# Kernel tuning notes

Measured on AMD Instinct MI355X. Metric: run time of the kernel, lower is better.

## Reference

```python
import jax, jax.numpy as jnp
import numpy as np

N = 8192
LAYER_WIDTHS = [32, 64, 32]
LAYER_CENTERS = [512, 512]


def setup_inputs() -> dict:
    key = jax.random.key(0)
    ks = jax.random.split(key, 8)
    inp = {"x": jax.random.normal(ks[0], (N, LAYER_WIDTHS[0]), dtype=jnp.float32)}
    # layer 0 params
    inp["centers0"] = jax.random.normal(ks[1], (LAYER_CENTERS[0], LAYER_WIDTHS[0]), dtype=jnp.float32)
    inp["log_sigmas0"] = jnp.zeros((LAYER_CENTERS[0],), dtype=jnp.float32)
    lim0 = 1.0 / np.sqrt(LAYER_CENTERS[0])
    inp["W0"] = jax.random.uniform(ks[2], (LAYER_WIDTHS[1], LAYER_CENTERS[0]), jnp.float32, -lim0, lim0)
    inp["b0"] = jax.random.uniform(ks[3], (LAYER_WIDTHS[1],), jnp.float32, -lim0, lim0)
    # layer 1 params
    inp["centers1"] = jax.random.normal(ks[4], (LAYER_CENTERS[1], LAYER_WIDTHS[1]), dtype=jnp.float32)
    inp["log_sigmas1"] = jnp.zeros((LAYER_CENTERS[1],), dtype=jnp.float32)
    lim1 = 1.0 / np.sqrt(LAYER_CENTERS[1])
    inp["W1"] = jax.random.uniform(ks[5], (LAYER_WIDTHS[2], LAYER_CENTERS[1]), jnp.float32, -lim1, lim1)
    inp["b1"] = jax.random.uniform(ks[6], (LAYER_WIDTHS[2],), jnp.float32, -lim1, lim1)
    return inp


def _rbf(h, centers, log_sigmas):
    # h: [N, in], centers: [C, in] -> [N, C]
    diff = h[:, None, :] - centers[None, :, :]            # [N, C, in]
    dist = jnp.sqrt(jnp.sum(diff * diff, axis=-1))        # [N, C]
    d = dist / jnp.exp(log_sigmas)[None, :]
    return jnp.exp(-(d * d))                              # gaussian basis


def reference(x, centers0, log_sigmas0, W0, b0, centers1, log_sigmas1, W1, b1):
    h = _rbf(x, centers0, log_sigmas0) @ W0.T + b0        # [N, widths[1]]
    h = _rbf(h, centers1, log_sigmas1) @ W1.T + b1        # [N, widths[2]]
    return h
```

## Files before the change

kernel.cpp:

```cpp
#include <hip/hip_runtime.h>
#include <math.h>


#define NROWS 8192
#define BLOCK 512
#define GRID (NROWS / 16)

typedef __attribute__((ext_vector_type(8))) short short8;
typedef __attribute__((ext_vector_type(4))) float f32x4;

__device__ __forceinline__ short bf16t(float f) {
    return (short)(__float_as_uint(f) >> 16);
}

__global__ void prepack(const float* __restrict__ c0, const float* __restrict__ ls0,
                        const float* __restrict__ W0,
                        const float* __restrict__ c1, const float* __restrict__ ls1,
                        const float* __restrict__ W1,
                        unsigned short* __restrict__ wpc0, unsigned short* __restrict__ wpc1,
                        unsigned short* __restrict__ wpw0, unsigned short* __restrict__ wpw1,
                        float2* __restrict__ cniv0, float2* __restrict__ cniv1)
{
    const int i = blockIdx.x * 256 + threadIdx.x;
    if (i < 16384) {
        const int e = i & 7, l = (i >> 3) & 63, nt = i >> 9;
        const int c = nt * 16 + (l & 15), k = (l >> 4) * 8 + e;
        wpc0[i] = (unsigned short)bf16t(c0[c * 32 + k]);
    } else if (i < 49152) {
        const int j = i - 16384;
        const int e = j & 7, l = (j >> 3) & 63, kk = (j >> 9) & 1, nt = j >> 10;
        const int c = nt * 16 + (l & 15), k = kk * 32 + (l >> 4) * 8 + e;
        wpc1[j] = (unsigned short)bf16t(c1[c * 64 + k]);
    } else if (i < 81920) {
        const int j = i - 49152;
        const int e = j & 7, l = (j >> 3) & 63, nt = (j >> 9) & 3, ks = j >> 11;
        const int col = nt * 16 + (l & 15), k = ks * 32 + (l >> 4) * 8 + e;
        wpw0[j] = (unsigned short)bf16t(W0[col * 512 + k]);
    } else if (i < 98304) {
        const int j = i - 81920;
        const int e = j & 7, l = (j >> 3) & 63, nt = (j >> 9) & 1, ks = j >> 10;
        const int col = nt * 16 + (l & 15), k = ks * 32 + (l >> 4) * 8 + e;
        wpw1[j] = (unsigned short)bf16t(W1[col * 512 + k]);
    } else if (i < 98304 + 512) {
        const int c = i - 98304;
        float s = 0.f;
        for (int d = 0; d < 32; ++d) { const float v = c0[c * 32 + d]; s += v * v; }
        cniv0[c] = make_float2(s, __expf(-2.0f * ls0[c]));
    } else if (i < 98304 + 1024) {
        const int c = i - 98816;
        float s = 0.f;
        for (int d = 0; d < 64; ++d) { const float v = c1[c * 64 + d]; s += v * v; }
        cniv1[c] = make_float2(s, __expf(-2.0f * ls1[c]));
    }
}

__global__ __launch_bounds__(BLOCK, 4)
void rbfnet(const float* __restrict__ x,
            const float* __restrict__ b0, const float* __restrict__ b1,
            const unsigned short* __restrict__ wpc0, const unsigned short* __restrict__ wpc1,
            const unsigned short* __restrict__ wpw0, const unsigned short* __restrict__ wpw1,
            const float2* __restrict__ cniv0, const float2* __restrict__ cniv1,
            float* __restrict__ out)
{
    __shared__ unsigned short phi_u[16 * 520];
    __shared__ unsigned short hfrag[16 * 72];
    __shared__ float htmp[2][16][68];
    __shared__ float otmp[4][16][36];
    __shared__ float hn_lds[16];

    const int t  = threadIdx.x;
    const int l  = t & 63;
    const int w  = t >> 6;
    const int mr = l & 15;
    const int kg = l >> 4;
    const int row0 = blockIdx.x * 16;

    short8 ax;
    float rnv[4];
    {
        const float4 x0 = *(const float4*)&x[(row0 + mr) * 32 + kg * 8];
        const float4 x1 = *(const float4*)&x[(row0 + mr) * 32 + kg * 8 + 4];
        const float xo[8] = {x0.x, x0.y, x0.z, x0.w, x1.x, x1.y, x1.z, x1.w};
        float rp = 0.f;
        #pragma unroll
        for (int i = 0; i < 8; ++i) { ax[i] = bf16t(xo[i]); rp += xo[i] * xo[i]; }
        rp += __shfl_xor(rp, 16);
        rp += __shfl_xor(rp, 32);
        #pragma unroll
        for (int g = 0; g < 4; ++g) rnv[g] = __shfl(rp, 4 * kg + g);
    }

    {
        #pragma unroll 2
        for (int q = 0; q < 4; ++q) {
            const int nt = 4 * w + q;
            const int c  = nt * 16 + mr;
            const short8 bc = *(const short8*)&wpc0[(nt * 64 + l) * 8];
            const float2 cv = cniv0[c];
            f32x4 d = {0.f, 0.f, 0.f, 0.f};
            d = __builtin_amdgcn_mfma_f32_16x16x32_bf16(ax, bc, d, 0, 0, 0);
            #pragma unroll
            for (int g = 0; g < 4; ++g) {
                const float p = __expf(-(rnv[g] + cv.x - 2.f * d[g]) * cv.y);
                phi_u[(4 * kg + g) * 520 + c] = (unsigned short)bf16t(p);
            }
        }
    }
    __syncthreads();

    {
        const int nt = w & 3, half = w >> 2;
        f32x4 hD = {0.f, 0.f, 0.f, 0.f};
        #pragma unroll 2
        for (int ks = 8 * half; ks < 8 * half + 8; ++ks) {
            const short8 ap = *(const short8*)&phi_u[mr * 520 + ks * 32 + kg * 8];
            const short8 bw = *(const short8*)&wpw0[((ks * 4 + nt) * 64 + l) * 8];
            hD = __builtin_amdgcn_mfma_f32_16x16x32_bf16(ap, bw, hD, 0, 0, 0);
        }
        #pragma unroll
        for (int g = 0; g < 4; ++g) htmp[half][4 * kg + g][nt * 16 + mr] = hD[g];
    }
    __syncthreads();

    {
        const int r = t >> 5, dd = t & 31;
        const float h0 = htmp[0][r][dd]      + htmp[1][r][dd]      + b0[dd];
        const float h1 = htmp[0][r][dd + 32] + htmp[1][r][dd + 32] + b0[dd + 32];
        hfrag[r * 72 + dd]      = (unsigned short)bf16t(h0);
        hfrag[r * 72 + 32 + dd] = (unsigned short)bf16t(h1);
        float s = h0 * h0 + h1 * h1;
        s += __shfl_xor(s, 1);  s += __shfl_xor(s, 2);  s += __shfl_xor(s, 4);
        s += __shfl_xor(s, 8);  s += __shfl_xor(s, 16);
        if (dd == 0) hn_lds[r] = s;
    }
    __syncthreads();

    {
        const short8 ah0 = *(const short8*)&hfrag[mr * 72 + kg * 8];
        const short8 ah1 = *(const short8*)&hfrag[mr * 72 + 32 + kg * 8];
        float hnv[4];
        #pragma unroll
        for (int g = 0; g < 4; ++g) hnv[g] = hn_lds[4 * kg + g];
        #pragma unroll 2
        for (int q = 0; q < 4; ++q) {
            const int nt = 4 * w + q;
            const int c  = nt * 16 + mr;
            const short8 bc0 = *(const short8*)&wpc1[((nt * 2 + 0) * 64 + l) * 8];
            const short8 bc1 = *(const short8*)&wpc1[((nt * 2 + 1) * 64 + l) * 8];
            const float2 cv = cniv1[c];
            f32x4 d = {0.f, 0.f, 0.f, 0.f};
            d = __builtin_amdgcn_mfma_f32_16x16x32_bf16(ah0, bc0, d, 0, 0, 0);
            d = __builtin_amdgcn_mfma_f32_16x16x32_bf16(ah1, bc1, d, 0, 0, 0);
            #pragma unroll
            for (int g = 0; g < 4; ++g) {
                const float p = __expf(-(hnv[g] + cv.x - 2.f * d[g]) * cv.y);
                phi_u[(4 * kg + g) * 520 + c] = (unsigned short)bf16t(p);
            }
        }
    }
    __syncthreads();

    {
        const int nt = w & 1, qtr = w >> 1;
        f32x4 oD = {0.f, 0.f, 0.f, 0.f};
        #pragma unroll 2
        for (int ks = 4 * qtr; ks < 4 * qtr + 4; ++ks) {
            const short8 ap = *(const short8*)&phi_u[mr * 520 + ks * 32 + kg * 8];
            const short8 bw = *(const short8*)&wpw1[((ks * 2 + nt) * 64 + l) * 8];
            oD = __builtin_amdgcn_mfma_f32_16x16x32_bf16(ap, bw, oD, 0, 0, 0);
        }
        #pragma unroll
        for (int g = 0; g < 4; ++g) otmp[qtr][4 * kg + g][nt * 16 + mr] = oD[g];
    }
    __syncthreads();

    {
        const int r = t >> 5, j = t & 31;
        const float s = otmp[0][r][j] + otmp[1][r][j] + otmp[2][r][j] + otmp[3][r][j] + b1[j];
        out[(row0 + r) * 32 + j] = s;
    }
}

extern "C" void kernel_launch(void* const* d_in, const int* in_sizes, int n_in,
                              void* d_out, int out_size, void* d_ws, size_t ws_size,
                              hipStream_t stream) {
    const float* xin = (const float*)d_in[0];
    const float* c0  = (const float*)d_in[1];
    const float* ls0 = (const float*)d_in[2];
    const float* W0  = (const float*)d_in[3];
    const float* b0  = (const float*)d_in[4];
    const float* c1  = (const float*)d_in[5];
    const float* ls1 = (const float*)d_in[6];
    const float* W1  = (const float*)d_in[7];
    const float* b1  = (const float*)d_in[8];
    float* outp = (float*)d_out;

    char* ws = (char*)d_ws;
    unsigned short* wpc0 = (unsigned short*)(ws);
    unsigned short* wpc1 = (unsigned short*)(ws + 32768);
    unsigned short* wpw0 = (unsigned short*)(ws + 98304);
    unsigned short* wpw1 = (unsigned short*)(ws + 163840);
    float2* cniv0 = (float2*)(ws + 196608);
    float2* cniv1 = (float2*)(ws + 200704);

    hipLaunchKernelGGL(prepack, dim3(388), dim3(256), 0, stream,
                       c0, ls0, W0, c1, ls1, W1, wpc0, wpc1, wpw0, wpw1, cniv0, cniv1);
    hipLaunchKernelGGL(rbfnet, dim3(GRID), dim3(BLOCK), 0, stream,
                       xin, b0, b1, wpc0, wpc1, wpw0, wpw1, cniv0, cniv1, outp);
}
```

Baseline: 79.08 us.

## Process 32 rows per block, drop split-K reductions, vectorize weight prepack

```diff
diff --git a/kernel.cpp b/kernel.cpp
--- a/kernel.cpp
+++ b/kernel.cpp
@@ -3,14 +3,18 @@
 
 
 #define NROWS 8192
+#define ROWS 32
 #define BLOCK 512
-#define GRID (NROWS / 16)
+#define GRID (NROWS / ROWS)
 
 typedef __attribute__((ext_vector_type(8))) short short8;
 typedef __attribute__((ext_vector_type(4))) float f32x4;
 
 __device__ __forceinline__ short bf16t(float f) {
     return (short)(__float_as_uint(f) >> 16);
+}
+__device__ __forceinline__ float bf16f(short u) {
+    return __uint_as_float(((unsigned)(unsigned short)u) << 16);
 }
 
 __global__ void prepack(const float* __restrict__ c0, const float* __restrict__ ls0,
@@ -21,40 +25,65 @@
                         unsigned short* __restrict__ wpw0, unsigned short* __restrict__ wpw1,
                         float2* __restrict__ cniv0, float2* __restrict__ cniv1)
 {
-    const int i = blockIdx.x * 256 + threadIdx.x;
-    if (i < 16384) {
-        const int e = i & 7, l = (i >> 3) & 63, nt = i >> 9;
-        const int c = nt * 16 + (l & 15), k = (l >> 4) * 8 + e;
-        wpc0[i] = (unsigned short)bf16t(c0[c * 32 + k]);
-    } else if (i < 49152) {
-        const int j = i - 16384;
-        const int e = j & 7, l = (j >> 3) & 63, kk = (j >> 9) & 1, nt = j >> 10;
-        const int c = nt * 16 + (l & 15), k = kk * 32 + (l >> 4) * 8 + e;
-        wpc1[j] = (unsigned short)bf16t(c1[c * 64 + k]);
-    } else if (i < 81920) {
-        const int j = i - 49152;
-        const int e = j & 7, l = (j >> 3) & 63, nt = (j >> 9) & 3, ks = j >> 11;
-        const int col = nt * 16 + (l & 15), k = ks * 32 + (l >> 4) * 8 + e;
-        wpw0[j] = (unsigned short)bf16t(W0[col * 512 + k]);
-    } else if (i < 98304) {
-        const int j = i - 81920;
-        const int e = j & 7, l = (j >> 3) & 63, nt = (j >> 9) & 1, ks = j >> 10;
-        const int col = nt * 16 + (l & 15), k = ks * 32 + (l >> 4) * 8 + e;
-        wpw1[j] = (unsigned short)bf16t(W1[col * 512 + k]);
-    } else if (i < 98304 + 512) {
-        const int c = i - 98304;
-        float s = 0.f;
-        for (int d = 0; d < 32; ++d) { const float v = c0[c * 32 + d]; s += v * v; }
-        cniv0[c] = make_float2(s, __expf(-2.0f * ls0[c]));
-    } else if (i < 98304 + 1024) {
-        const int c = i - 98816;
-        float s = 0.f;
-        for (int d = 0; d < 64; ++d) { const float v = c1[c * 64 + d]; s += v * v; }
-        cniv1[c] = make_float2(s, __expf(-2.0f * ls1[c]));
-    }
-}
-
-__global__ __launch_bounds__(BLOCK, 4)
+    const int b  = blockIdx.x;
+    const int gi = b * 256 + threadIdx.x;
+    const int l  = gi & 63, mr = l & 15, kg = l >> 4;
+
+    if (b < 8) {
+        const int nt = gi >> 6;
+        const float4 v0 = *(const float4*)&c0[(nt * 16 + mr) * 32 + kg * 8];
+        const float4 v1 = *(const float4*)&c0[(nt * 16 + mr) * 32 + kg * 8 + 4];
+        const float o[8] = {v0.x, v0.y, v0.z, v0.w, v1.x, v1.y, v1.z, v1.w};
+        short8 p; float rp = 0.f;
+        #pragma unroll
+        for (int i = 0; i < 8; ++i) { p[i] = bf16t(o[i]); rp += o[i] * o[i]; }
+        *(short8*)&wpc0[(nt * 64 + l) * 8] = p;
+        rp += __shfl_xor(rp, 16);
+        rp += __shfl_xor(rp, 32);
+        if (kg == 0)
+            cniv0[nt * 16 + mr] = make_float2(rp, __expf(-2.0f * ls0[nt * 16 + mr]));
+    } else if (b < 16) {
+        const int i2 = gi - 2048;
+        const int nt = i2 >> 6;
+        float rp = 0.f;
+        #pragma unroll
+        for (int kk = 0; kk < 2; ++kk) {
+            const float4 v0 = *(const float4*)&c1[(nt * 16 + mr) * 64 + kk * 32 + kg * 8];
+            const float4 v1 = *(const float4*)&c1[(nt * 16 + mr) * 64 + kk * 32 + kg * 8 + 4];
+            const float o[8] = {v0.x, v0.y, v0.z, v0.w, v1.x, v1.y, v1.z, v1.w};
+            short8 p;
+            #pragma unroll
+            for (int i = 0; i < 8; ++i) { p[i] = bf16t(o[i]); rp += o[i] * o[i]; }
+            *(short8*)&wpc1[((nt * 2 + kk) * 64 + l) * 8] = p;
+        }
+        rp += __shfl_xor(rp, 16);
+        rp += __shfl_xor(rp, 32);
+        if (kg == 0)
+            cniv1[nt * 16 + mr] = make_float2(rp, __expf(-2.0f * ls1[nt * 16 + mr]));
+    } else if (b < 32) {
+        const int i2 = gi - 4096;
+        const int nt = (i2 >> 6) & 3, ks = i2 >> 8;
+        const float4 v0 = *(const float4*)&W0[(nt * 16 + mr) * 512 + ks * 32 + kg * 8];
+        const float4 v1 = *(const float4*)&W0[(nt * 16 + mr) * 512 + ks * 32 + kg * 8 + 4];
+        const float o[8] = {v0.x, v0.y, v0.z, v0.w, v1.x, v1.y, v1.z, v1.w};
+        short8 p;
+        #pragma unroll
+        for (int i = 0; i < 8; ++i) p[i] = bf16t(o[i]);
+        *(short8*)&wpw0[((ks * 4 + nt) * 64 + l) * 8] = p;
+    } else {
+        const int i2 = gi - 8192;
+        const int nt = (i2 >> 6) & 1, ks = i2 >> 7;
+        const float4 v0 = *(const float4*)&W1[(nt * 16 + mr) * 512 + ks * 32 + kg * 8];
+        const float4 v1 = *(const float4*)&W1[(nt * 16 + mr) * 512 + ks * 32 + kg * 8 + 4];
+        const float o[8] = {v0.x, v0.y, v0.z, v0.w, v1.x, v1.y, v1.z, v1.w};
+        short8 p;
+        #pragma unroll
+        for (int i = 0; i < 8; ++i) p[i] = bf16t(o[i]);
+        *(short8*)&wpw1[((ks * 2 + nt) * 64 + l) * 8] = p;
+    }
+}
+
+__global__ __launch_bounds__(BLOCK, 2)
 void rbfnet(const float* __restrict__ x,
             const float* __restrict__ b0, const float* __restrict__ b1,
             const unsigned short* __restrict__ wpc0, const unsigned short* __restrict__ wpc1,
@@ -62,32 +91,32 @@
             const float2* __restrict__ cniv0, const float2* __restrict__ cniv1,
             float* __restrict__ out)
 {
-    __shared__ unsigned short phi_u[16 * 520];
-    __shared__ unsigned short hfrag[16 * 72];
-    __shared__ float htmp[2][16][68];
-    __shared__ float otmp[4][16][36];
-    __shared__ float hn_lds[16];
+    __shared__ unsigned short phi_u[32 * 520];
+    __shared__ unsigned short hfrag[32 * 72];
 
     const int t  = threadIdx.x;
     const int l  = t & 63;
     const int w  = t >> 6;
     const int mr = l & 15;
     const int kg = l >> 4;
-    const int row0 = blockIdx.x * 16;
-
-    short8 ax;
-    float rnv[4];
-    {
-        const float4 x0 = *(const float4*)&x[(row0 + mr) * 32 + kg * 8];
-        const float4 x1 = *(const float4*)&x[(row0 + mr) * 32 + kg * 8 + 4];
+    const int row0 = blockIdx.x * ROWS;
+
+    short8 ax0, ax1;
+    float rnv[2][4];
+    #pragma unroll
+    for (int mt = 0; mt < 2; ++mt) {
+        const float4 x0 = *(const float4*)&x[(row0 + mt * 16 + mr) * 32 + kg * 8];
+        const float4 x1 = *(const float4*)&x[(row0 + mt * 16 + mr) * 32 + kg * 8 + 4];
         const float xo[8] = {x0.x, x0.y, x0.z, x0.w, x1.x, x1.y, x1.z, x1.w};
         float rp = 0.f;
-        #pragma unroll
-        for (int i = 0; i < 8; ++i) { ax[i] = bf16t(xo[i]); rp += xo[i] * xo[i]; }
+        short8 a;
+        #pragma unroll
+        for (int i = 0; i < 8; ++i) { a[i] = bf16t(xo[i]); rp += xo[i] * xo[i]; }
+        if (mt == 0) ax0 = a; else ax1 = a;
         rp += __shfl_xor(rp, 16);
         rp += __shfl_xor(rp, 32);
         #pragma unroll
-        for (int g = 0; g < 4; ++g) rnv[g] = __shfl(rp, 4 * kg + g);
+        for (int g = 0; g < 4; ++g) rnv[mt][g] = __shfl(rp, 4 * kg + g);
     }
 
     {
@@ -97,50 +126,56 @@
             const int c  = nt * 16 + mr;
             const short8 bc = *(const short8*)&wpc0[(nt * 64 + l) * 8];
             const float2 cv = cniv0[c];
-            f32x4 d = {0.f, 0.f, 0.f, 0.f};
-            d = __builtin_amdgcn_mfma_f32_16x16x32_bf16(ax, bc, d, 0, 0, 0);
+            f32x4 d0 = {0.f, 0.f, 0.f, 0.f}, d1 = {0.f, 0.f, 0.f, 0.f};
+            d0 = __builtin_amdgcn_mfma_f32_16x16x32_bf16(ax0, bc, d0, 0, 0, 0);
+            d1 = __builtin_amdgcn_mfma_f32_16x16x32_bf16(ax1, bc, d1, 0, 0, 0);
             #pragma unroll
             for (int g = 0; g < 4; ++g) {
-                const float p = __expf(-(rnv[g] + cv.x - 2.f * d[g]) * cv.y);
-                phi_u[(4 * kg + g) * 520 + c] = (unsigned short)bf16t(p);
+                phi_u[(4 * kg + g) * 520 + c] =
+                    (unsigned short)bf16t(__expf(-(rnv[0][g] + cv.x - 2.f * d0[g]) * cv.y));
+                phi_u[(16 + 4 * kg + g) * 520 + c] =
+                    (unsigned short)bf16t(__expf(-(rnv[1][g] + cv.x - 2.f * d1[g]) * cv.y));
             }
         }
     }
     __syncthreads();
 
     {
-        const int nt = w & 3, half = w >> 2;
+        const int nt = w & 3, mt = w >> 2;
         f32x4 hD = {0.f, 0.f, 0.f, 0.f};
-        #pragma unroll 2
-        for (int ks = 8 * half; ks < 8 * half + 8; ++ks) {
-            const short8 ap = *(const short8*)&phi_u[mr * 520 + ks * 32 + kg * 8];
+        #pragma unroll 4
+        for (int ks = 0; ks < 16; ++ks) {
+            const short8 ap = *(const short8*)&phi_u[(mt * 16 + mr) * 520 + ks * 32 + kg * 8];
             const short8 bw = *(const short8*)&wpw0[((ks * 4 + nt) * 64 + l) * 8];
             hD = __builtin_amdgcn_mfma_f32_16x16x32_bf16(ap, bw, hD, 0, 0, 0);
         }
-        #pragma unroll
-        for (int g = 0; g < 4; ++g) htmp[half][4 * kg + g][nt * 16 + mr] = hD[g];
+        const float bj = b0[nt * 16 + mr];
+        #pragma unroll
+        for (int g = 0; g < 4; ++g)
+            hfrag[(mt * 16 + 4 * kg + g) * 72 + nt * 16 + mr] =
+                (unsigned short)bf16t(hD[g] + bj);
     }
     __syncthreads();
 
     {
-        const int r = t >> 5, dd = t & 31;
-        const float h0 = htmp[0][r][dd]      + htmp[1][r][dd]      + b0[dd];
-        const float h1 = htmp[0][r][dd + 32] + htmp[1][r][dd + 32] + b0[dd + 32];
-        hfrag[r * 72 + dd]      = (unsigned short)bf16t(h0);
-        hfrag[r * 72 + 32 + dd] = (unsigned short)bf16t(h1);
-        float s = h0 * h0 + h1 * h1;
-        s += __shfl_xor(s, 1);  s += __shfl_xor(s, 2);  s += __shfl_xor(s, 4);
-        s += __shfl_xor(s, 8);  s += __shfl_xor(s, 16);
-        if (dd == 0) hn_lds[r] = s;
-    }
-    __syncthreads();
-
-    {
-        const short8 ah0 = *(const short8*)&hfrag[mr * 72 + kg * 8];
-        const short8 ah1 = *(const short8*)&hfrag[mr * 72 + 32 + kg * 8];
-        float hnv[4];
-        #pragma unroll
-        for (int g = 0; g < 4; ++g) hnv[g] = hn_lds[4 * kg + g];
+        short8 ah00, ah01, ah10, ah11;
+        float hnv[2][4];
+        #pragma unroll
+        for (int mt = 0; mt < 2; ++mt) {
+            const short8 a0 = *(const short8*)&hfrag[(mt * 16 + mr) * 72 + kg * 8];
+            const short8 a1 = *(const short8*)&hfrag[(mt * 16 + mr) * 72 + 32 + kg * 8];
+            if (mt == 0) { ah00 = a0; ah01 = a1; } else { ah10 = a0; ah11 = a1; }
+            float rp = 0.f;
+            #pragma unroll
+            for (int i = 0; i < 8; ++i) {
+                const float v0 = bf16f(a0[i]), v1 = bf16f(a1[i]);
+                rp += v0 * v0 + v1 * v1;
+            }
+            rp += __shfl_xor(rp, 16);
+            rp += __shfl_xor(rp, 32);
+            #pragma unroll
+            for (int g = 0; g < 4; ++g) hnv[mt][g] = __shfl(rp, 4 * kg + g);
+        }
         #pragma unroll 2
         for (int q = 0; q < 4; ++q) {
             const int nt = 4 * w + q;
@@ -148,36 +183,35 @@
             const short8 bc0 = *(const short8*)&wpc1[((nt * 2 + 0) * 64 + l) * 8];
             const short8 bc1 = *(const short8*)&wpc1[((nt * 2 + 1) * 64 + l) * 8];
             const float2 cv = cniv1[c];
-            f32x4 d = {0.f, 0.f, 0.f, 0.f};
-            d = __builtin_amdgcn_mfma_f32_16x16x32_bf16(ah0, bc0, d, 0, 0, 0);
-            d = __builtin_amdgcn_mfma_f32_16x16x32_bf16(ah1, bc1, d, 0, 0, 0);
+            f32x4 d0 = {0.f, 0.f, 0.f, 0.f}, d1 = {0.f, 0.f, 0.f, 0.f};
+            d0 = __builtin_amdgcn_mfma_f32_16x16x32_bf16(ah00, bc0, d0, 0, 0, 0);
+            d0 = __builtin_amdgcn_mfma_f32_16x16x32_bf16(ah01, bc1, d0, 0, 0, 0);
+            d1 = __builtin_amdgcn_mfma_f32_16x16x32_bf16(ah10, bc0, d1, 0, 0, 0);
+            d1 = __builtin_amdgcn_mfma_f32_16x16x32_bf16(ah11, bc1, d1, 0, 0, 0);
             #pragma unroll
             for (int g = 0; g < 4; ++g) {
-                const float p = __expf(-(hnv[g] + cv.x - 2.f * d[g]) * cv.y);
-                phi_u[(4 * kg + g) * 520 + c] = (unsigned short)bf16t(p);
+                phi_u[(4 * kg + g) * 520 + c] =
+                    (unsigned short)bf16t(__expf(-(hnv[0][g] + cv.x - 2.f * d0[g]) * cv.y));
+                phi_u[(16 + 4 * kg + g) * 520 + c] =
+                    (unsigned short)bf16t(__expf(-(hnv[1][g] + cv.x - 2.f * d1[g]) * cv.y));
             }
         }
     }
     __syncthreads();
 
-    {
-        const int nt = w & 1, qtr = w >> 1;
+    if (w < 4) {
+        const int nt = w & 1, mt = w >> 1;
         f32x4 oD = {0.f, 0.f, 0.f, 0.f};
-        #pragma unroll 2
-        for (int ks = 4 * qtr; ks < 4 * qtr + 4; ++ks) {
-            const short8 ap = *(const short8*)&phi_u[mr * 520 + ks * 32 + kg * 8];
+        #pragma unroll 4
+        for (int ks = 0; ks < 16; ++ks) {
+            const short8 ap = *(const short8*)&phi_u[(mt * 16 + mr) * 520 + ks * 32 + kg * 8];
             const short8 bw = *(const short8*)&wpw1[((ks * 2 + nt) * 64 + l) * 8];
             oD = __builtin_amdgcn_mfma_f32_16x16x32_bf16(ap, bw, oD, 0, 0, 0);
         }
-        #pragma unroll
-        for (int g = 0; g < 4; ++g) otmp[qtr][4 * kg + g][nt * 16 + mr] = oD[g];
-    }
-    __syncthreads();
-
-    {
-        const int r = t >> 5, j = t & 31;
-        const float s = otmp[0][r][j] + otmp[1][r][j] + otmp[2][r][j] + otmp[3][r][j] + b1[j];
-        out[(row0 + r) * 32 + j] = s;
+        const float bj = b1[nt * 16 + mr];
+        #pragma unroll
+        for (int g = 0; g < 4; ++g)
+            out[(row0 + mt * 16 + 4 * kg + g) * 32 + nt * 16 + mr] = oD[g] + bj;
     }
 }
 
@@ -203,7 +237,7 @@
     float2* cniv0 = (float2*)(ws + 196608);
     float2* cniv1 = (float2*)(ws + 200704);
 
-    hipLaunchKernelGGL(prepack, dim3(388), dim3(256), 0, stream,
+    hipLaunchKernelGGL(prepack, dim3(40), dim3(256), 0, stream,
                        c0, ls0, W0, c1, ls1, W1, wpc0, wpc1, wpw0, wpw1, cniv0, cniv1);
     hipLaunchKernelGGL(rbfnet, dim3(GRID), dim3(BLOCK), 0, stream,
                        xin, b0, b1, wpc0, wpc1, wpw0, wpw1, cniv0, cniv1, outp);
```

After: 77.90 us. Within noise of the previous version (-1.5%).
